# Optimization experiments

Measured on AMD Instinct MI355X. Metric: run time of the kernel, lower is better.

## Reference

```python
import jax, jax.numpy as jnp
import numpy as np

HIDDEN = 2048
N_HEADS = 16
N_KV = 2
HEAD_DIM = 256
ROT_DIM = 64  # partial_rotary_factor 0.25
EPS = 1e-6
B, S = 2, 2048


def _rms_norm(x, w, eps=EPS):
    var = jnp.mean(jnp.square(x), axis=-1, keepdims=True)
    return x * jax.lax.rsqrt(var + eps) * w


def _rotate_half(x):
    x1, x2 = jnp.split(x, 2, axis=-1)
    return jnp.concatenate([-x2, x1], axis=-1)


def setup_inputs() -> dict:
    key = jax.random.key(0)
    ks = jax.random.split(key, 8)
    hidden_states = jax.random.normal(ks[0], (B, S, HIDDEN), dtype=jnp.float32)
    # real RoPE cos/sin over rotary_dim (HF convention: freqs duplicated)
    inv_freq = 1.0 / (10000.0 ** (np.arange(0, ROT_DIM, 2, dtype=np.float32) / ROT_DIM))
    pos = np.arange(S, dtype=np.float32)
    ang = np.einsum('s,f->sf', pos, inv_freq)                # [S, ROT_DIM/2]
    emb = np.concatenate([ang, ang], axis=-1)                # [S, ROT_DIM]
    cos = jnp.asarray(np.broadcast_to(np.cos(emb), (B, S, ROT_DIM)))
    sin = jnp.asarray(np.broadcast_to(np.sin(emb), (B, S, ROT_DIM)))
    sc = 0.02
    Wq = jax.random.normal(ks[1], (N_HEADS * HEAD_DIM * 2, HIDDEN), dtype=jnp.float32) * sc
    Wk = jax.random.normal(ks[2], (N_KV * HEAD_DIM, HIDDEN), dtype=jnp.float32) * sc
    Wv = jax.random.normal(ks[3], (N_KV * HEAD_DIM, HIDDEN), dtype=jnp.float32) * sc
    Wo = jax.random.normal(ks[4], (HIDDEN, N_HEADS * HEAD_DIM), dtype=jnp.float32) * sc
    q_norm_w = jnp.ones((HEAD_DIM,), dtype=jnp.float32)
    k_norm_w = jnp.ones((HEAD_DIM,), dtype=jnp.float32)
    return {"hidden_states": hidden_states, "cos": cos, "sin": sin,
            "Wq": Wq, "Wk": Wk, "Wv": Wv, "Wo": Wo,
            "q_norm_w": q_norm_w, "k_norm_w": k_norm_w}


def reference(hidden_states, cos, sin, Wq, Wk, Wv, Wo, q_norm_w, k_norm_w):
    b, s, _ = hidden_states.shape
    # gated Q projection: [b, s, n_heads, 2*head_dim] -> query, gate
    qg = jnp.einsum('bsd,od->bso', hidden_states, Wq).reshape(b, s, N_HEADS, 2 * HEAD_DIM)
    q, gate = jnp.split(qg, 2, axis=-1)                      # each [b,s,H,D]
    gate = gate.reshape(b, s, N_HEADS * HEAD_DIM)
    k = jnp.einsum('bsd,od->bso', hidden_states, Wk).reshape(b, s, N_KV, HEAD_DIM)
    v = jnp.einsum('bsd,od->bso', hidden_states, Wv).reshape(b, s, N_KV, HEAD_DIM)
    # per-head RMSNorm before RoPE
    q = _rms_norm(q, q_norm_w)
    k = _rms_norm(k, k_norm_w)
    # partial RoPE on first ROT_DIM dims
    c = cos[:, :, None, :]
    sn = sin[:, :, None, :]
    q_rot, q_pass = q[..., :ROT_DIM], q[..., ROT_DIM:]
    k_rot, k_pass = k[..., :ROT_DIM], k[..., ROT_DIM:]
    q_rot = q_rot * c + _rotate_half(q_rot) * sn
    k_rot = k_rot * c + _rotate_half(k_rot) * sn
    q = jnp.concatenate([q_rot, q_pass], axis=-1)
    k = jnp.concatenate([k_rot, k_pass], axis=-1)
    # GQA: repeat kv heads
    rep = N_HEADS // N_KV
    k = jnp.repeat(k, rep, axis=2)
    v = jnp.repeat(v, rep, axis=2)
    scale = 1.0 / jnp.sqrt(jnp.float32(HEAD_DIM))
    scores = jnp.einsum('bqhd,bkhd->bhqk', q, k) * scale
    causal = jnp.tril(jnp.ones((s, s), dtype=bool))
    scores = jnp.where(causal[None, None], scores, jnp.finfo(scores.dtype).min)
    probs = jax.nn.softmax(scores, axis=-1)
    attn = jnp.einsum('bhqk,bkhd->bqhd', probs, v).reshape(b, s, N_HEADS * HEAD_DIM)
    attn = attn * jax.nn.sigmoid(gate)
    return jnp.einsum('bsi,oi->bso', attn, Wo)
```

## Files before the change

kernel.cpp:

```cpp
#include <hip/hip_runtime.h>
#include <stdint.h>

typedef unsigned short u16;
typedef __bf16 bf16x8 __attribute__((ext_vector_type(8)));
typedef float f32x4 __attribute__((ext_vector_type(4)));
typedef u16 u16x4 __attribute__((ext_vector_type(4)));
typedef u16 u16x8 __attribute__((ext_vector_type(8)));

__device__ __forceinline__ u16 f2b(float f) {
    unsigned u = __builtin_bit_cast(unsigned, f);
    u = u + 0x7FFFu + ((u >> 16) & 1u);
    return (u16)(u >> 16);
}
__device__ __forceinline__ float b2f(u16 b) {
    return __builtin_bit_cast(float, (unsigned)b << 16);
}

__device__ __forceinline__ void glds16(const u16* g, u16* l) {
    __builtin_amdgcn_global_load_lds(
        (const __attribute__((address_space(1))) void*)g,
        (__attribute__((address_space(3))) void*)l,
        16, 0, 0);
}

template <int N> __device__ __forceinline__ void waitvm() {
    if constexpr (N == 0)      asm volatile("s_waitcnt vmcnt(0)" ::: "memory");
    else if constexpr (N == 3) asm volatile("s_waitcnt vmcnt(3)" ::: "memory");
    else if constexpr (N == 4) asm volatile("s_waitcnt vmcnt(4)" ::: "memory");
    else if constexpr (N == 6) asm volatile("s_waitcnt vmcnt(6)" ::: "memory");
    else if constexpr (N == 8) asm volatile("s_waitcnt vmcnt(8)" ::: "memory");
}

__global__ __launch_bounds__(256) void cast_bf16(const float* __restrict__ src,
                                                 u16* __restrict__ dst, int n) {
    int i = (blockIdx.x * 256 + threadIdx.x) * 4;
    if (i >= n) return;
    f32x4 v = *(const f32x4*)(src + i);
    u16x4 o;
    o.x = f2b(v.x); o.y = f2b(v.y); o.z = f2b(v.z); o.w = f2b(v.w);
    *(u16x4*)(dst + i) = o;
}

template <int OUT_BF16>
__global__ __launch_bounds__(256) void gemm_bt(const u16* __restrict__ A,
                                               const u16* __restrict__ Bt,
                                               void* __restrict__ Cout,
                                               int M, int N, int K) {
    __shared__ u16 As[128 * 32];
    __shared__ u16 Bs[128 * 32];
    const int tid  = threadIdx.x;
    const int w    = tid >> 6;
    const int lane = tid & 63;
    const int quad = lane >> 4;
    const int ml   = lane & 15;
    const long bm  = (long)blockIdx.y * 128;
    const long bn  = (long)blockIdx.x * 128;
    const int wm   = (w >> 1) * 64;
    const int wn   = (w & 1) * 64;
    const int grow = lane >> 2;
    const int gcol = (lane & 3) * 8;

    const u16* Ag = A  + (bm + w * 16 + grow) * (long)K + gcol;
    const u16* Bg = Bt + (bn + w * 16 + grow) * (long)K + gcol;
    u16* lAs0 = &As[(w * 16) * 32];
    u16* lAs1 = &As[(64 + w * 16) * 32];
    u16* lBs0 = &Bs[(w * 16) * 32];
    u16* lBs1 = &Bs[(64 + w * 16) * 32];

    const f32x4 fz = {0.f, 0.f, 0.f, 0.f};
    f32x4 acc[4][4];
#pragma unroll
    for (int i = 0; i < 4; ++i)
#pragma unroll
        for (int j = 0; j < 4; ++j) acc[i][j] = fz;

    for (int k0 = 0; k0 < K; k0 += 32) {
        __syncthreads();
        glds16(Ag + k0,                lAs0);
        glds16(Ag + 64 * (long)K + k0, lAs1);
        glds16(Bg + k0,                lBs0);
        glds16(Bg + 64 * (long)K + k0, lBs1);
        __builtin_amdgcn_s_waitcnt(0);
        __syncthreads();
        bf16x8 af[4], bfr[4];
#pragma unroll
        for (int mt = 0; mt < 4; ++mt)
            af[mt] = *(const bf16x8*)&As[(wm + mt * 16 + ml) * 32 + quad * 8];
#pragma unroll
        for (int nt = 0; nt < 4; ++nt)
            bfr[nt] = *(const bf16x8*)&Bs[(wn + nt * 16 + ml) * 32 + quad * 8];
#pragma unroll
        for (int mt = 0; mt < 4; ++mt)
#pragma unroll
            for (int nt = 0; nt < 4; ++nt)
                acc[mt][nt] = __builtin_amdgcn_mfma_f32_16x16x32_bf16(
                    af[mt], bfr[nt], acc[mt][nt], 0, 0, 0);
    }
#pragma unroll
    for (int mt = 0; mt < 4; ++mt)
#pragma unroll
        for (int nt = 0; nt < 4; ++nt)
#pragma unroll
            for (int r = 0; r < 4; ++r) {
                long row = bm + wm + mt * 16 + quad * 4 + r;
                long col = bn + wn + nt * 16 + ml;
                float v = acc[mt][nt][r];
                if (OUT_BF16) ((u16*)Cout)[row * N + col] = f2b(v);
                else          ((float*)Cout)[row * N + col] = v;
            }
}

template <int OUT_BF16, int BN>
__global__ __launch_bounds__(512, 2) void gemm256(const u16* __restrict__ A,
                                                  const u16* __restrict__ Bt,
                                                  void* __restrict__ Cout,
                                                  int M, int N, int K, int nbx) {
    (void)M;
    constexpr int NFRAG = BN / 64;
    constexpr int ASZ = 256 * 32;
    constexpr int BSZ = BN * 32;
    constexpr int LPT = (BN == 256) ? 4 : 3;
    __shared__ u16 sm[4][ASZ + BSZ];

    const int tid  = threadIdx.x;
    const int w    = tid >> 6;
    const int lane = tid & 63;
    const int quad = lane >> 4;
    const int ml   = lane & 15;
    const int wm   = (w >> 2) * 128;
    const int wn   = (w & 3) * (BN / 4);

    const int nwg = gridDim.x;
    const int q8 = nwg >> 3, r8 = nwg & 7;
    const int xcd = blockIdx.x & 7, loc = blockIdx.x >> 3;
    const int wg  = (xcd < r8 ? xcd * (q8 + 1) : r8 * (q8 + 1) + (xcd - r8) * q8) + loc;
    const long bm = (long)(wg / nbx) * 256;
    const long bn = (long)(wg % nbx) * BN;

    const int  srow = w * 16 + (lane >> 2);
    const int  scc  = (lane & 3) ^ ((lane >> 3) & 3);
    const u16* Ag0  = A  + (bm + srow) * (long)K + scc * 8;
    const u16* Ag1  = Ag0 + 128 * (long)K;
    const u16* Bg0  = Bt + (bn + srow) * (long)K + scc * 8;
    const u16* Bg1  = (BN == 256) ? Bg0 + 128 * (long)K : Bg0;
    const int  ldsw = w * 512;

    const int ccr  = quad ^ ((ml >> 1) & 3);
    const int aoff = (wm + ml) * 32 + ccr * 8;
    const int boff = (wn + ml) * 32 + ccr * 8;

    const f32x4 fz = {0.f, 0.f, 0.f, 0.f};
    f32x4 acc[8][NFRAG];
#pragma unroll
    for (int i = 0; i < 8; ++i)
#pragma unroll
        for (int j = 0; j < NFRAG; ++j) acc[i][j] = fz;

    const int NT = K >> 5;

#define STAGE(tt)                                                      \
    {                                                                  \
        u16* base = &sm[(tt) & 3][0];                                  \
        const long ko = (long)(tt) * 32;                               \
        glds16(Ag0 + ko, base + ldsw);                                 \
        glds16(Ag1 + ko, base + 4096 + ldsw);                          \
        glds16(Bg0 + ko, base + ASZ + ldsw);                           \
        if (BN == 256) glds16(Bg1 + ko, base + ASZ + 4096 + ldsw);     \
    }

    STAGE(0); STAGE(1); STAGE(2);

    for (int t = 0; t < NT; ++t) {
        if (t < NT - 2)       waitvm<2 * LPT>();
        else if (t == NT - 2) waitvm<LPT>();
        else                  waitvm<0>();
        __builtin_amdgcn_s_barrier();
        __builtin_amdgcn_sched_barrier(0);
        if (t + 3 < NT) STAGE(t + 3);

        const u16* Ab = &sm[t & 3][0];
        const u16* Bb = Ab + ASZ;
        bf16x8 af[8];
#pragma unroll
        for (int mt = 0; mt < 8; ++mt)
            af[mt] = *(const bf16x8*)(Ab + aoff + mt * 512);
#pragma unroll
        for (int nh = 0; nh < NFRAG / 2; ++nh) {
            bf16x8 b0 = *(const bf16x8*)(Bb + boff + (2 * nh + 0) * 512);
            bf16x8 b1 = *(const bf16x8*)(Bb + boff + (2 * nh + 1) * 512);
            __builtin_amdgcn_s_setprio(1);
#pragma unroll
            for (int mt = 0; mt < 8; ++mt) {
                acc[mt][2 * nh]     = __builtin_amdgcn_mfma_f32_16x16x32_bf16(
                    af[mt], b0, acc[mt][2 * nh], 0, 0, 0);
                acc[mt][2 * nh + 1] = __builtin_amdgcn_mfma_f32_16x16x32_bf16(
                    af[mt], b1, acc[mt][2 * nh + 1], 0, 0, 0);
            }
            __builtin_amdgcn_s_setprio(0);
        }
    }
#undef STAGE

#pragma unroll
    for (int mt = 0; mt < 8; ++mt)
#pragma unroll
        for (int nt = 0; nt < NFRAG; ++nt)
#pragma unroll
            for (int r = 0; r < 4; ++r) {
                long row = bm + wm + mt * 16 + quad * 4 + r;
                long col = bn + wn + nt * 16 + ml;
                float v = acc[mt][nt][r];
                if (OUT_BF16) ((u16*)Cout)[row * N + col] = f2b(v);
                else          ((float*)Cout)[row * N + col] = v;
            }
}

__global__ __launch_bounds__(64) void norm_rope(const u16* __restrict__ qgk,
                                                const float* __restrict__ cosp,
                                                const float* __restrict__ sinp,
                                                const float* __restrict__ qw,
                                                const float* __restrict__ kw,
                                                u16* __restrict__ qf,
                                                u16* __restrict__ kf) {
    const int t = blockIdx.x;
    const int u = blockIdx.y;
    const int lane = threadIdx.x;
    const int b = t >> 11, s = t & 2047;
    const u16* src; const float* wgt; u16* dst;
    if (u < 16) {
        src = qgk + (long)t * 8704 + u * 512;
        wgt = qw;
        dst = qf + ((long)(b * 16 + u) * 2048 + s) * 256;
    } else {
        int kh = u - 16;
        src = qgk + (long)t * 8704 + 8192 + kh * 256;
        wgt = kw;
        dst = kf + ((long)(b * 2 + kh) * 2048 + s) * 256;
    }
    const int d0 = lane * 4;
    u16x4 raw = *(const u16x4*)(src + d0);
    float x0 = b2f(raw.x), x1 = b2f(raw.y), x2 = b2f(raw.z), x3 = b2f(raw.w);
    float ss = x0 * x0 + x1 * x1 + x2 * x2 + x3 * x3;
    for (int off = 32; off; off >>= 1) ss += __shfl_xor(ss, off, 64);
    float inv = rsqrtf(ss * (1.0f / 256.0f) + 1e-6f);
    float n0 = x0 * inv * wgt[d0 + 0];
    float n1 = x1 * inv * wgt[d0 + 1];
    float n2 = x2 * inv * wgt[d0 + 2];
    float n3 = x3 * inv * wgt[d0 + 3];
    float p0 = __shfl_xor(n0, 8, 64);
    float p1 = __shfl_xor(n1, 8, 64);
    float p2 = __shfl_xor(n2, 8, 64);
    float p3 = __shfl_xor(n3, 8, 64);
    if (lane < 16) {
        f32x4 c  = *(const f32x4*)(cosp + (long)t * 64 + d0);
        f32x4 sn = *(const f32x4*)(sinp + (long)t * 64 + d0);
        float sgn = (lane < 8) ? -1.f : 1.f;
        n0 = n0 * c[0] + sgn * p0 * sn[0];
        n1 = n1 * c[1] + sgn * p1 * sn[1];
        n2 = n2 * c[2] + sgn * p2 * sn[2];
        n3 = n3 * c[3] + sgn * p3 * sn[3];
    }
    const float qs = (u < 16) ? 0.0625f : 1.0f;
    n0 *= qs; n1 *= qs; n2 *= qs; n3 *= qs;
    u16x4 o;
    o.x = f2b(n0); o.y = f2b(n1); o.z = f2b(n2); o.w = f2b(n3);
    *(u16x4*)(dst + d0) = o;
}

__global__ __launch_bounds__(256) void attn_fused(const u16* __restrict__ qf,
                                                  const u16* __restrict__ kf,
                                                  const u16* __restrict__ vt,
                                                  const u16* __restrict__ qgk,
                                                  u16* __restrict__ attn_g) {
    __shared__ u16 Ks[64 * 256];
    __shared__ u16 Vt[256 * 64];
    __shared__ u16 P[64 * 64];
    const int flat = blockIdx.x;
    const int qt = 31 - (flat >> 5);
    const int h  = flat & 15;
    const int b  = (flat >> 4) & 1;
    const int kh = h >> 3;
    const int tid = threadIdx.x;
    const int w = tid >> 6, lane = tid & 63;
    const int quad = lane >> 4, ml = lane & 15;
    const int qrow = qt * 64 + w * 16;

    const u16* qptr = qf + ((long)(b * 16 + h) * 2048 + qrow + ml) * 256;
    bf16x8 qfrag[8];
#pragma unroll
    for (int dd = 0; dd < 8; ++dd)
        qfrag[dd] = *(const bf16x8*)(qptr + dd * 32 + quad * 8);

    const f32x4 fz = {0.f, 0.f, 0.f, 0.f};
    f32x4 oacc[16];
#pragma unroll
    for (int i = 0; i < 16; ++i) oacc[i] = fz;
    float lsum[4] = {0.f, 0.f, 0.f, 0.f};

    const u16* kbp = kf + (long)(b * 2 + kh) * 2048 * 256;
    const u16* vbp = vt + (long)kh * 256 * 4096 + (long)b * 2048;

    const int krow = tid >> 5;
    const int kswz = (tid & 31) ^ krow;
    const int vrow = tid >> 3;
    const int vswz = (tid & 7) ^ (vrow & 7);
    u16* ldsKw = &Ks[w * 512];
    u16* ldsVw = &Vt[w * 512];

    const int m7 = ml & 7;

    const int nkt = qt + 1;
    for (int kt = 0; kt < nkt; ++kt) {
        const int kb = kt * 64;
        __syncthreads();
#pragma unroll
        for (int i = 0; i < 8; ++i)
            glds16(kbp + (long)(kb + i * 8 + krow) * 256 + kswz * 8,
                   ldsKw + i * 2048);
#pragma unroll
        for (int i = 0; i < 8; ++i)
            glds16(vbp + (long)(i * 32 + vrow) * 4096 + kb + vswz * 8,
                   ldsVw + i * 2048);
        waitvm<8>();
        __builtin_amdgcn_s_barrier();
        __builtin_amdgcn_sched_barrier(0);

        f32x4 sacc[4];
#pragma unroll
        for (int i = 0; i < 4; ++i) sacc[i] = fz;
#pragma unroll
        for (int dd = 0; dd < 8; ++dd) {
            const int ck = (dd * 4 + quad) ^ m7;
            bf16x8 kf0 = *(const bf16x8*)&Ks[(0 * 16 + ml) * 256 + ck * 8];
            bf16x8 kf1 = *(const bf16x8*)&Ks[(1 * 16 + ml) * 256 + ck * 8];
            bf16x8 kf2 = *(const bf16x8*)&Ks[(2 * 16 + ml) * 256 + ck * 8];
            bf16x8 kf3 = *(const bf16x8*)&Ks[(3 * 16 + ml) * 256 + ck * 8];
            __builtin_amdgcn_s_setprio(1);
            sacc[0] = __builtin_amdgcn_mfma_f32_16x16x32_bf16(qfrag[dd], kf0, sacc[0], 0, 0, 0);
            sacc[1] = __builtin_amdgcn_mfma_f32_16x16x32_bf16(qfrag[dd], kf1, sacc[1], 0, 0, 0);
            sacc[2] = __builtin_amdgcn_mfma_f32_16x16x32_bf16(qfrag[dd], kf2, sacc[2], 0, 0, 0);
            sacc[3] = __builtin_amdgcn_mfma_f32_16x16x32_bf16(qfrag[dd], kf3, sacc[3], 0, 0, 0);
            __builtin_amdgcn_s_setprio(0);
        }

        const bool diag = (kt == qt);
#pragma unroll
        for (int nt = 0; nt < 4; ++nt)
#pragma unroll
            for (int r = 0; r < 4; ++r) {
                float sv = sacc[nt][r];
                const int row = w * 16 + quad * 4 + r;
                if (diag) {
                    int col = nt * 16 + ml;
                    sv = (col > (quad * 4 + r + w * 16)) ? -1e30f : sv;
                }
                float pv = __expf(sv - 16.0f);
                lsum[r] += pv;
                const int chk = (nt * 2 + (ml >> 3)) ^ ((quad * 4 + r) & 7);
                P[row * 64 + chk * 8 + m7] = f2b(pv);
            }

        waitvm<0>();
        __builtin_amdgcn_s_barrier();
        __builtin_amdgcn_sched_barrier(0);

#pragma unroll
        for (int ks = 0; ks < 2; ++ks) {
            const int ck = (ks * 4 + quad) ^ m7;
            bf16x8 pfrag = *(const bf16x8*)&P[(w * 16 + ml) * 64 + ck * 8];
            __builtin_amdgcn_s_setprio(1);
#pragma unroll
            for (int dt = 0; dt < 16; ++dt) {
                bf16x8 vfrag = *(const bf16x8*)&Vt[(dt * 16 + ml) * 64 + ck * 8];
                oacc[dt] = __builtin_amdgcn_mfma_f32_16x16x32_bf16(pfrag, vfrag, oacc[dt], 0, 0, 0);
            }
            __builtin_amdgcn_s_setprio(0);
        }
    }

#pragma unroll
    for (int off = 1; off < 16; off <<= 1)
#pragma unroll
        for (int r = 0; r < 4; ++r) lsum[r] += __shfl_xor(lsum[r], off, 64);

#pragma unroll
    for (int dt = 0; dt < 16; ++dt)
#pragma unroll
        for (int r = 0; r < 4; ++r) {
            int srow = qrow + quad * 4 + r;
            long tok = (long)b * 2048 + srow;
            int d = dt * 16 + ml;
            float o = oacc[dt][r] / lsum[r];
            float g = b2f(qgk[tok * 8704 + h * 512 + 256 + d]);
            float gv = o / (1.f + __expf(-g));
            attn_g[tok * 4096 + h * 256 + d] = f2b(gv);
        }
}

extern "C" void kernel_launch(void* const* d_in, const int* in_sizes, int n_in,
                              void* d_out, int out_size, void* d_ws, size_t ws_size,
                              hipStream_t stream) {
    (void)in_sizes; (void)n_in; (void)out_size;
    const float* hidden = (const float*)d_in[0];
    const float* cosp   = (const float*)d_in[1];
    const float* sinp   = (const float*)d_in[2];
    const float* Wq     = (const float*)d_in[3];
    const float* Wk     = (const float*)d_in[4];
    const float* Wv     = (const float*)d_in[5];
    const float* Wo     = (const float*)d_in[6];
    const float* qw     = (const float*)d_in[7];
    const float* kw     = (const float*)d_in[8];
    float* out = (float*)d_out;

    char* p = (char*)d_ws;
    u16* h_bf   = (u16*)p; p += (size_t)8388608 * 2;
    u16* Wqk_bf = (u16*)p; p += (size_t)17825792 * 2;
    u16* Wv_bf  = (u16*)p; p += (size_t)1048576 * 2;
    u16* Wo_bf  = (u16*)p; p += (size_t)8388608 * 2;
    u16* qgk    = (u16*)p; p += (size_t)35651584 * 2;
    u16* v_t    = (u16*)p; p += (size_t)2097152 * 2;
    u16* q_f    = (u16*)p; p += (size_t)16777216 * 2;
    u16* k_f    = (u16*)p; p += (size_t)2097152 * 2;
    u16* attn_g = (u16*)p; p += (size_t)16777216 * 2;
    if ((size_t)(p - (char*)d_ws) > ws_size) return;

    cast_bf16<<<8192,  256, 0, stream>>>(hidden, h_bf, 8388608);
    cast_bf16<<<16384, 256, 0, stream>>>(Wq, Wqk_bf, 16777216);
    cast_bf16<<<1024,  256, 0, stream>>>(Wk, Wqk_bf + (size_t)8192 * 2048, 1048576);
    cast_bf16<<<1024,  256, 0, stream>>>(Wv, Wv_bf, 1048576);
    cast_bf16<<<8192,  256, 0, stream>>>(Wo, Wo_bf, 8388608);

    gemm256<1, 256><<<dim3(544), 512, 0, stream>>>(h_bf, Wqk_bf, qgk, 4096, 8704, 2048, 34);
    gemm_bt<1><<<dim3(32, 4), 256, 0, stream>>>(Wv_bf, h_bf, v_t, 512, 4096, 2048);

    norm_rope<<<dim3(4096, 18), 64, 0, stream>>>(qgk, cosp, sinp, qw, kw, q_f, k_f);

    attn_fused<<<dim3(1024), 256, 0, stream>>>(q_f, k_f, v_t, qgk, attn_g);

    gemm256<0, 128><<<dim3(256), 512, 0, stream>>>(attn_g, Wo_bf, out, 4096, 2048, 4096, 16);
}
```

Before: 596.5 us.

## Shrink GEMM M-tile to 128 with double-buffered LDS and more resident blocks

Replaces the 256-row, 4-stage GEMM with a 128-row tile, 2-stage LDS buffer and launch bounds allowing 4 blocks per CU. Fragments are loaded into registers before a second barrier, after which the next stage's load is issued, so the buffer can be refilled while MFMAs run. Both the QKV and output projections launch twice as many workgroups. The aim is higher occupancy and better wave/CU balance, at the cost of less per-block data reuse and extra barriers per K-step.

New measurement: 608.5 us. +2.0%, slower.

```diff
diff --git a/kernel.cpp b/kernel.cpp
--- a/kernel.cpp
+++ b/kernel.cpp
@@ -25,6 +25,7 @@
 
 template <int N> __device__ __forceinline__ void waitvm() {
     if constexpr (N == 0)      asm volatile("s_waitcnt vmcnt(0)" ::: "memory");
+    else if constexpr (N == 2) asm volatile("s_waitcnt vmcnt(2)" ::: "memory");
     else if constexpr (N == 3) asm volatile("s_waitcnt vmcnt(3)" ::: "memory");
     else if constexpr (N == 4) asm volatile("s_waitcnt vmcnt(4)" ::: "memory");
     else if constexpr (N == 6) asm volatile("s_waitcnt vmcnt(6)" ::: "memory");
@@ -111,36 +112,35 @@
 }
 
 template <int OUT_BF16, int BN>
-__global__ __launch_bounds__(512, 2) void gemm256(const u16* __restrict__ A,
-                                                  const u16* __restrict__ Bt,
-                                                  void* __restrict__ Cout,
-                                                  int M, int N, int K, int nbx) {
+__global__ __launch_bounds__(512, 4) void gemm_pipe(const u16* __restrict__ A,
+                                                    const u16* __restrict__ Bt,
+                                                    void* __restrict__ Cout,
+                                                    int M, int N, int K, int nbx) {
     (void)M;
-    constexpr int NFRAG = BN / 64;
-    constexpr int ASZ = 256 * 32;
+    constexpr int NF  = BN / 64;
+    constexpr int ASZ = 128 * 32;
     constexpr int BSZ = BN * 32;
-    constexpr int LPT = (BN == 256) ? 4 : 3;
-    __shared__ u16 sm[4][ASZ + BSZ];
+    constexpr int LPT = 1 + BN / 128;
+    __shared__ u16 sm[2][ASZ + BSZ];
 
     const int tid  = threadIdx.x;
     const int w    = tid >> 6;
     const int lane = tid & 63;
     const int quad = lane >> 4;
     const int ml   = lane & 15;
-    const int wm   = (w >> 2) * 128;
+    const int wm   = (w >> 2) * 64;
     const int wn   = (w & 3) * (BN / 4);
 
     const int nwg = gridDim.x;
     const int q8 = nwg >> 3, r8 = nwg & 7;
     const int xcd = blockIdx.x & 7, loc = blockIdx.x >> 3;
     const int wg  = (xcd < r8 ? xcd * (q8 + 1) : r8 * (q8 + 1) + (xcd - r8) * q8) + loc;
-    const long bm = (long)(wg / nbx) * 256;
+    const long bm = (long)(wg / nbx) * 128;
     const long bn = (long)(wg % nbx) * BN;
 
     const int  srow = w * 16 + (lane >> 2);
     const int  scc  = (lane & 3) ^ ((lane >> 3) & 3);
     const u16* Ag0  = A  + (bm + srow) * (long)K + scc * 8;
-    const u16* Ag1  = Ag0 + 128 * (long)K;
     const u16* Bg0  = Bt + (bn + srow) * (long)K + scc * 8;
     const u16* Bg1  = (BN == 256) ? Bg0 + 128 * (long)K : Bg0;
     const int  ldsw = w * 512;
@@ -150,61 +150,61 @@
     const int boff = (wn + ml) * 32 + ccr * 8;
 
     const f32x4 fz = {0.f, 0.f, 0.f, 0.f};
-    f32x4 acc[8][NFRAG];
-#pragma unroll
-    for (int i = 0; i < 8; ++i)
-#pragma unroll
-        for (int j = 0; j < NFRAG; ++j) acc[i][j] = fz;
+    f32x4 acc[4][NF];
+#pragma unroll
+    for (int i = 0; i < 4; ++i)
+#pragma unroll
+        for (int j = 0; j < NF; ++j) acc[i][j] = fz;
 
     const int NT = K >> 5;
 
 #define STAGE(tt)                                                      \
     {                                                                  \
-        u16* base = &sm[(tt) & 3][0];                                  \
+        u16* base = &sm[(tt) & 1][0];                                  \
         const long ko = (long)(tt) * 32;                               \
         glds16(Ag0 + ko, base + ldsw);                                 \
-        glds16(Ag1 + ko, base + 4096 + ldsw);                          \
         glds16(Bg0 + ko, base + ASZ + ldsw);                           \
         if (BN == 256) glds16(Bg1 + ko, base + ASZ + 4096 + ldsw);     \
     }
 
-    STAGE(0); STAGE(1); STAGE(2);
+    STAGE(0); STAGE(1);
 
     for (int t = 0; t < NT; ++t) {
-        if (t < NT - 2)       waitvm<2 * LPT>();
-        else if (t == NT - 2) waitvm<LPT>();
-        else                  waitvm<0>();
+        if (t + 1 < NT) waitvm<LPT>();
+        else            waitvm<0>();
         __builtin_amdgcn_s_barrier();
         __builtin_amdgcn_sched_barrier(0);
-        if (t + 3 < NT) STAGE(t + 3);
-
-        const u16* Ab = &sm[t & 3][0];
+
+        const u16* Ab = &sm[t & 1][0];
         const u16* Bb = Ab + ASZ;
-        bf16x8 af[8];
-#pragma unroll
-        for (int mt = 0; mt < 8; ++mt)
+        bf16x8 af[4], bfr[NF];
+#pragma unroll
+        for (int mt = 0; mt < 4; ++mt)
             af[mt] = *(const bf16x8*)(Ab + aoff + mt * 512);
 #pragma unroll
-        for (int nh = 0; nh < NFRAG / 2; ++nh) {
-            bf16x8 b0 = *(const bf16x8*)(Bb + boff + (2 * nh + 0) * 512);
-            bf16x8 b1 = *(const bf16x8*)(Bb + boff + (2 * nh + 1) * 512);
-            __builtin_amdgcn_s_setprio(1);
-#pragma unroll
-            for (int mt = 0; mt < 8; ++mt) {
-                acc[mt][2 * nh]     = __builtin_amdgcn_mfma_f32_16x16x32_bf16(
-                    af[mt], b0, acc[mt][2 * nh], 0, 0, 0);
-                acc[mt][2 * nh + 1] = __builtin_amdgcn_mfma_f32_16x16x32_bf16(
-                    af[mt], b1, acc[mt][2 * nh + 1], 0, 0, 0);
-            }
-            __builtin_amdgcn_s_setprio(0);
-        }
+        for (int nt = 0; nt < NF; ++nt)
+            bfr[nt] = *(const bf16x8*)(Bb + boff + nt * 512);
+
+        asm volatile("s_waitcnt lgkmcnt(0)" ::: "memory");
+        __builtin_amdgcn_sched_barrier(0);
+        __builtin_amdgcn_s_barrier();
+        if (t + 2 < NT) STAGE(t + 2);
+
+        __builtin_amdgcn_s_setprio(1);
+#pragma unroll
+        for (int mt = 0; mt < 4; ++mt)
+#pragma unroll
+            for (int nt = 0; nt < NF; ++nt)
+                acc[mt][nt] = __builtin_amdgcn_mfma_f32_16x16x32_bf16(
+                    af[mt], bfr[nt], acc[mt][nt], 0, 0, 0);
+        __builtin_amdgcn_s_setprio(0);
     }
 #undef STAGE
 
 #pragma unroll
-    for (int mt = 0; mt < 8; ++mt)
-#pragma unroll
-        for (int nt = 0; nt < NFRAG; ++nt)
+    for (int mt = 0; mt < 4; ++mt)
+#pragma unroll
+        for (int nt = 0; nt < NF; ++nt)
 #pragma unroll
             for (int r = 0; r < 4; ++r) {
                 long row = bm + wm + mt * 16 + quad * 4 + r;
@@ -430,12 +430,12 @@
     cast_bf16<<<1024,  256, 0, stream>>>(Wv, Wv_bf, 1048576);
     cast_bf16<<<8192,  256, 0, stream>>>(Wo, Wo_bf, 8388608);
 
-    gemm256<1, 256><<<dim3(544), 512, 0, stream>>>(h_bf, Wqk_bf, qgk, 4096, 8704, 2048, 34);
+    gemm_pipe<1, 256><<<dim3(1088), 512, 0, stream>>>(h_bf, Wqk_bf, qgk, 4096, 8704, 2048, 34);
     gemm_bt<1><<<dim3(32, 4), 256, 0, stream>>>(Wv_bf, h_bf, v_t, 512, 4096, 2048);
 
     norm_rope<<<dim3(4096, 18), 64, 0, stream>>>(qgk, cosp, sinp, qw, kw, q_f, k_f);
 
     attn_fused<<<dim3(1024), 256, 0, stream>>>(q_f, k_f, v_t, qgk, attn_g);
 
-    gemm256<0, 128><<<dim3(256), 512, 0, stream>>>(attn_g, Wo_bf, out, 4096, 2048, 4096, 16);
-}
+    gemm_pipe<0, 128><<<dim3(512), 512, 0, stream>>>(attn_g, Wo_bf, out, 4096, 2048, 4096, 16);
+}
```
